# Performance work log

Measured on AMD Instinct MI355X. Metric: run time of the kernel, lower is better.

## Reference

```python
import jax, jax.numpy as jnp
import numpy as np


def setup_inputs() -> dict:
    key = jax.random.key(0)
    L, N, Q, C = 6, 64, 64, 256
    hs_pair = jax.random.normal(key, (L, N, Q, C), dtype=jnp.float32)
    return {"hs_pair": hs_pair}


def _merge_step(centers):
    # centers: [L, N, Q, C] -> [L, N, Q-1, C]
    L, N, Q, C = centers.shape
    # pairwise Euclidean distance via gram matrix (avoids [L,N,Q,Q,C] diff tensor)
    sq = jnp.sum(centers * centers, axis=-1)                      # [L,N,Q]
    gram = jnp.einsum('lnqc,lnpc->lnqp', centers, centers)        # [L,N,Q,Q]
    d2 = sq[..., :, None] + sq[..., None, :] - 2.0 * gram
    dist = jnp.sqrt(jnp.maximum(d2, 0.0))                         # [L,N,Q,Q]
    dist = dist + jnp.max(dist) * jnp.eye(Q, dtype=dist.dtype)
    idx = jnp.argmin(dist.reshape(L, N, Q * Q), axis=2)           # [L,N]
    x, y = idx // Q, idx % Q                                      # row-major argmin => x < y
    cx = jnp.take_along_axis(centers, x[:, :, None, None], axis=2)[:, :, 0]  # [L,N,C]
    cy = jnp.take_along_axis(centers, y[:, :, None, None], axis=2)[:, :, 0]  # [L,N,C]
    merged = (cx + cy) * 0.5
    last = centers[:, :, -1]                                      # [L,N,C]
    qr = jnp.arange(Q)
    mask_x = (qr[None, None, :] == x[:, :, None])[..., None]      # [L,N,Q,1]
    mask_y = (qr[None, None, :] == y[:, :, None])[..., None]
    centers = jnp.where(mask_x, merged[:, :, None, :], centers)
    centers = jnp.where(mask_y, last[:, :, None, :], centers)
    return centers[:, :, :-1]


def reference(hs_pair):
    centers = hs_pair
    Q0 = centers.shape[2]
    # Q-2 sequential merges; each iteration has a distinct static shape,
    # so a Python loop (unrolled under jit) is the correct structure.
    for _ in range(Q0 - 2):
        centers = _merge_step(centers)
    return centers  # [L, N, 2, C]
```

## Files before the change

### kernel.cpp

```cpp
#include <hip/hip_runtime.h>
#include <stdint.h>

#define NSLICE 384
#define QMAX   64
#define CDIM   256
#define NTHR   512

#define SW(r,c) ((r)*QMAX + ((c)^(r)))
#define INF_F  __int_as_float(0x7F800000)

__device__ __forceinline__ float dpp_sum64(float v) {
#define DPP_ADD(c) v += __int_as_float(__builtin_amdgcn_update_dpp(0, __float_as_int(v), c, 0xf, 0xf, true))
    DPP_ADD(0x111);
    DPP_ADD(0x112);
    DPP_ADD(0x114);
    DPP_ADD(0x118);
    DPP_ADD(0x142);
    DPP_ADD(0x143);
#undef DPP_ADD
    return v;
}

template<int CTRL>
__device__ __forceinline__ unsigned long long dpp_min64_step(unsigned long long v) {
    unsigned lo = (unsigned)v, hi = (unsigned)(v >> 32);
    unsigned olo = (unsigned)__builtin_amdgcn_update_dpp((int)lo, (int)lo, CTRL, 0xf, 0xf, false);
    unsigned ohi = (unsigned)__builtin_amdgcn_update_dpp((int)hi, (int)hi, CTRL, 0xf, 0xf, false);
    unsigned long long o = ((unsigned long long)ohi << 32) | olo;
    return o < v ? o : v;
}

__device__ __forceinline__ unsigned long long wave_min64_bcast(unsigned long long v) {
    v = dpp_min64_step<0x111>(v);
    v = dpp_min64_step<0x112>(v);
    v = dpp_min64_step<0x114>(v);
    v = dpp_min64_step<0x118>(v);
    v = dpp_min64_step<0x142>(v);
    v = dpp_min64_step<0x143>(v);
    unsigned lo = (unsigned)__builtin_amdgcn_readlane((int)(unsigned)v, 63);
    unsigned hi = (unsigned)__builtin_amdgcn_readlane((int)(unsigned)(v >> 32), 63);
    return ((unsigned long long)hi << 32) | lo;
}

__launch_bounds__(NTHR, 4)
__global__ void hca_kernel(const float* __restrict__ in, float* __restrict__ out) {
    __shared__ __align__(16) float cen[QMAX * CDIM];
    __shared__ __align__(16) float dist[QMAX * QMAX];

    const int tid  = threadIdx.x;
    const int lane = tid & 63;
    const int w    = tid >> 6;
    const int slice = blockIdx.x;
    const float* src = in + (size_t)slice * (QMAX * CDIM);
    float* dst = out + (size_t)slice * (2 * CDIM);

    {
        const float4* s4 = (const float4*)src;
        float4* c4 = (float4*)cen;
        #pragma unroll
        for (int i = 0; i < (QMAX * CDIM / 4) / NTHR; ++i)
            c4[tid + i * NTHR] = s4[tid + i * NTHR];
    }
    __syncthreads();

    {
        float4 A[8];
        #pragma unroll
        for (int r = 0; r < 8; ++r)
            A[r] = ((const float4*)(cen + (w + 8 * r) * CDIM))[lane];

        #pragma unroll
        for (int r = 0; r < 8; ++r) {
            float t = A[r].x * A[r].x;
            t = fmaf(A[r].y, A[r].y, t); t = fmaf(A[r].z, A[r].z, t); t = fmaf(A[r].w, A[r].w, t);
            float s = dpp_sum64(t);
            if (lane == 63) dist[(w + 8 * r) * QMAX] = s;
        }
        __syncthreads();

        float sqq[8];
        #pragma unroll
        for (int r = 0; r < 8; ++r) sqq[r] = dist[(w + 8 * r) * QMAX];
        for (int p = 1; p < QMAX; ++p) {
            const float4 b = ((const float4*)(cen + p * CDIM))[lane];
            const float sqp = dist[p * QMAX];
            #pragma unroll
            for (int r = 0; r < 8; ++r) {
                const int q = w + 8 * r;
                if (q < p) {
                    float t = A[r].x * b.x;
                    t = fmaf(A[r].y, b.y, t); t = fmaf(A[r].z, b.z, t); t = fmaf(A[r].w, b.w, t);
                    float s = dpp_sum64(t);
                    if (lane == 63) {
                        float d2 = sqq[r] + sqp - 2.0f * s;
                        float d  = sqrtf(fmaxf(d2, 0.0f));
                        dist[SW(q, p)] = d;
                        dist[SW(p, q)] = d;
                    }
                }
            }
        }
    }
    __syncthreads();

    if (w != 0) return;

    auto scan_chunk = [&](int i, unsigned long long& kmin) {
        const float4 dv = ((const float4*)dist)[i * 64 + lane];
        const int rr  = 4 * i + (lane >> 4);
        const int rb  = rr * 64;
        const int cc0 = (lane & 15) * 4;
        #pragma unroll
        for (int e = 0; e < 4; ++e) {
            unsigned long long kk =
                ((unsigned long long)__float_as_uint((&dv.x)[e]) << 32)
                | (unsigned)(rb + ((cc0 + e) ^ rr));
            kmin = kk < kmin ? kk : kmin;
        }
    };

    unsigned long long kmin = ~0ull;
    #pragma unroll
    for (int i = 0; i < 16; ++i) scan_chunk(i, kmin);
    kmin = wave_min64_bcast(kmin);

    for (int Q = QMAX; Q > 2; --Q) {
        const int Qm1 = Q - 1;
        const unsigned fl = (unsigned)kmin & 0xFFFu;
        const int x = (int)(fl >> 6), y = (int)(fl & 63);
        const float dxy = __uint_as_float((unsigned)(kmin >> 32));

        const float4 cx  = ((const float4*)(cen + x * CDIM))[lane];
        const float4 cy4 = ((const float4*)(cen + y * CDIM))[lane];
        const float4 cq  = ((const float4*)(cen + Qm1 * CDIM))[lane];

        const int p = lane;
        const bool act = (p < Qm1) && (p != x);
        const int p_old = (p == y) ? Qm1 : p;
        float dxp = 0.0f, dyp = 0.0f;
        if (act) { dxp = dist[SW(x, p_old)]; dyp = dist[SW(y, p_old)]; }
        const bool mv = (y != Qm1) && (p < Qm1) && (p != x) && (p != y);
        float rowQ1 = 0.0f, colQ1 = 0.0f;
        if (mv) { rowQ1 = dist[SW(Qm1, p)]; colQ1 = dist[SW(p, Qm1)]; }
        float t = 0.5f * (dxp * dxp + dyp * dyp) - 0.25f * (dxy * dxy);
        float d = sqrtf(fmaxf(t, 0.0f));
        if (mv) { dist[SW(y, p)] = rowQ1; dist[SW(p, y)] = colQ1; }
        if (p < Q) { dist[SW(Qm1, p)] = INF_F; dist[SW(p, Qm1)] = INF_F; }
        if (act) { dist[SW(x, p)] = d; dist[SW(p, x)] = d; }

        float4 m;
        m.x = (cx.x + cy4.x) * 0.5f; m.y = (cx.y + cy4.y) * 0.5f;
        m.z = (cx.z + cy4.z) * 0.5f; m.w = (cx.w + cy4.w) * 0.5f;
        ((float4*)(cen + x * CDIM))[lane] = m;
        if (y != Qm1) ((float4*)(cen + y * CDIM))[lane] = cq;

        if (Q > 3) {
            const int nc = ((Q - 2) >> 2) + 1;
            kmin = ~0ull;
            for (int i = 0; i < nc; ++i) scan_chunk(i, kmin);
            kmin = wave_min64_bcast(kmin);
        }
    }

    #pragma unroll
    for (int i = 0; i < 2; ++i)
        ((float4*)dst)[lane + 64 * i] = ((const float4*)cen)[lane + 64 * i];
}

extern "C" void kernel_launch(void* const* d_in, const int* in_sizes, int n_in,
                              void* d_out, int out_size, void* d_ws, size_t ws_size,
                              hipStream_t stream) {
    (void)in_sizes; (void)n_in; (void)d_ws; (void)ws_size; (void)out_size;
    const float* in = (const float*)d_in[0];
    float* out = (float*)d_out;
    hca_kernel<<<NSLICE, NTHR, 0, stream>>>(in, out);
}
```

Measured before the change: 147.2 us.

## Maintain per-row minimum keys incrementally instead of rescanning distance matrix

Replaces the full rescan of the remaining distance matrix after each merge with a per-lane row-minimum cache (one row per lane). After a merge, each row's cached minimum is patched for the row move and the new merged distances. Only rows whose cached minimum pointed at the removed or merged columns are rescanned, using wave-wide reductions. This cuts the per-step LDS scan work, at the cost of more complex bookkeeping and several extra cross-lane reductions per step.

```diff
diff --git a/kernel.cpp b/kernel.cpp
--- a/kernel.cpp
+++ b/kernel.cpp
@@ -8,6 +8,7 @@
 
 #define SW(r,c) ((r)*QMAX + ((c)^(r)))
 #define INF_F  __int_as_float(0x7F800000)
+typedef unsigned long long ull;
 
 __device__ __forceinline__ float dpp_sum64(float v) {
 #define DPP_ADD(c) v += __int_as_float(__builtin_amdgcn_update_dpp(0, __float_as_int(v), c, 0xf, 0xf, true))
@@ -22,15 +23,15 @@
 }
 
 template<int CTRL>
-__device__ __forceinline__ unsigned long long dpp_min64_step(unsigned long long v) {
+__device__ __forceinline__ ull dpp_min64_step(ull v) {
     unsigned lo = (unsigned)v, hi = (unsigned)(v >> 32);
     unsigned olo = (unsigned)__builtin_amdgcn_update_dpp((int)lo, (int)lo, CTRL, 0xf, 0xf, false);
     unsigned ohi = (unsigned)__builtin_amdgcn_update_dpp((int)hi, (int)hi, CTRL, 0xf, 0xf, false);
-    unsigned long long o = ((unsigned long long)ohi << 32) | olo;
+    ull o = ((ull)ohi << 32) | olo;
     return o < v ? o : v;
 }
 
-__device__ __forceinline__ unsigned long long wave_min64_bcast(unsigned long long v) {
+__device__ __forceinline__ ull wave_min64_bcast(ull v) {
     v = dpp_min64_step<0x111>(v);
     v = dpp_min64_step<0x112>(v);
     v = dpp_min64_step<0x114>(v);
@@ -39,7 +40,7 @@
     v = dpp_min64_step<0x143>(v);
     unsigned lo = (unsigned)__builtin_amdgcn_readlane((int)(unsigned)v, 63);
     unsigned hi = (unsigned)__builtin_amdgcn_readlane((int)(unsigned)(v >> 32), 63);
-    return ((unsigned long long)hi << 32) | lo;
+    return ((ull)hi << 32) | lo;
 }
 
 __launch_bounds__(NTHR, 4)
@@ -105,30 +106,38 @@
 
     if (w != 0) return;
 
-    auto scan_chunk = [&](int i, unsigned long long& kmin) {
-        const float4 dv = ((const float4*)dist)[i * 64 + lane];
-        const int rr  = 4 * i + (lane >> 4);
-        const int rb  = rr * 64;
-        const int cc0 = (lane & 15) * 4;
-        #pragma unroll
-        for (int e = 0; e < 4; ++e) {
-            unsigned long long kk =
-                ((unsigned long long)__float_as_uint((&dv.x)[e]) << 32)
-                | (unsigned)(rb + ((cc0 + e) ^ rr));
-            kmin = kk < kmin ? kk : kmin;
-        }
-    };
-
-    unsigned long long kmin = ~0ull;
-    #pragma unroll
-    for (int i = 0; i < 16; ++i) scan_chunk(i, kmin);
-    kmin = wave_min64_bcast(kmin);
+    unsigned khi, klo;
+    {
+        ull acc[8];
+        #pragma unroll
+        for (int i = 0; i < 8; ++i) acc[i] = ~0ull;
+        #pragma unroll
+        for (int j = 0; j < 8; ++j) {
+            #pragma unroll
+            for (int i = 0; i < 8; ++i) {
+                const int c = 8 * j + i;
+                unsigned b = __float_as_uint(dist[SW(lane, c)]);
+                ull kk = ((ull)b << 32) | (unsigned)((lane << 6) | c);
+                acc[i] = kk < acc[i] ? kk : acc[i];
+            }
+        }
+        acc[0] = acc[0] < acc[4] ? acc[0] : acc[4];
+        acc[1] = acc[1] < acc[5] ? acc[1] : acc[5];
+        acc[2] = acc[2] < acc[6] ? acc[2] : acc[6];
+        acc[3] = acc[3] < acc[7] ? acc[3] : acc[7];
+        acc[0] = acc[0] < acc[2] ? acc[0] : acc[2];
+        acc[1] = acc[1] < acc[3] ? acc[1] : acc[3];
+        ull key = acc[0] < acc[1] ? acc[0] : acc[1];
+        khi = (unsigned)(key >> 32); klo = (unsigned)key;
+    }
+    ull kmin = wave_min64_bcast(((ull)khi << 32) | klo);
 
     for (int Q = QMAX; Q > 2; --Q) {
         const int Qm1 = Q - 1;
         const unsigned fl = (unsigned)kmin & 0xFFFu;
         const int x = (int)(fl >> 6), y = (int)(fl & 63);
         const float dxy = __uint_as_float((unsigned)(kmin >> 32));
+        const bool has_mv = (y != Qm1);
 
         const float4 cx  = ((const float4*)(cen + x * CDIM))[lane];
         const float4 cy4 = ((const float4*)(cen + y * CDIM))[lane];
@@ -139,7 +148,7 @@
         const int p_old = (p == y) ? Qm1 : p;
         float dxp = 0.0f, dyp = 0.0f;
         if (act) { dxp = dist[SW(x, p_old)]; dyp = dist[SW(y, p_old)]; }
-        const bool mv = (y != Qm1) && (p < Qm1) && (p != x) && (p != y);
+        const bool mv = has_mv && (p < Qm1) && (p != x) && (p != y);
         float rowQ1 = 0.0f, colQ1 = 0.0f;
         if (mv) { rowQ1 = dist[SW(Qm1, p)]; colQ1 = dist[SW(p, Qm1)]; }
         float t = 0.5f * (dxp * dxp + dyp * dyp) - 0.25f * (dxy * dxy);
@@ -152,13 +161,43 @@
         m.x = (cx.x + cy4.x) * 0.5f; m.y = (cx.y + cy4.y) * 0.5f;
         m.z = (cx.z + cy4.z) * 0.5f; m.w = (cx.w + cy4.w) * 0.5f;
         ((float4*)(cen + x * CDIM))[lane] = m;
-        if (y != Qm1) ((float4*)(cen + y * CDIM))[lane] = cq;
+        if (has_mv) ((float4*)(cen + y * CDIM))[lane] = cq;
 
         if (Q > 3) {
-            const int nc = ((Q - 2) >> 2) + 1;
-            kmin = ~0ull;
-            for (int i = 0; i < nc; ++i) scan_chunk(i, kmin);
-            kmin = wave_min64_bcast(kmin);
+            const int Qn = Q - 1;
+            unsigned rawcol = klo & 63u;
+            bool stale = (rawcol == (unsigned)x) | (rawcol == (unsigned)y);
+            unsigned fixcol = (has_mv && rawcol == (unsigned)Qm1) ? (unsigned)y : rawcol;
+            const unsigned inh_hi  = (unsigned)__builtin_amdgcn_readlane((int)khi, Qm1);
+            const unsigned inh_raw = (unsigned)__builtin_amdgcn_readlane((int)rawcol, Qm1);
+            if (has_mv && p == y) {
+                khi = inh_hi;
+                fixcol = inh_raw;
+                stale = (inh_raw == (unsigned)x) | (inh_raw == (unsigned)y);
+            }
+            klo = (unsigned)(p << 6) | fixcol;
+            if (act && !stale) {
+                const unsigned db = __float_as_uint(d);
+                const unsigned cl = (unsigned)((p << 6) | x);
+                if ((db < khi) | ((db == khi) & (cl < klo))) { khi = db; klo = cl; }
+            }
+            {
+                const unsigned h = act ? __float_as_uint(d) : 0xFFFFFFFFu;
+                ull kx = ((ull)h << 32) | (unsigned)((x << 6) | p);
+                kx = wave_min64_bcast(kx);
+                if (p == x) { khi = (unsigned)(kx >> 32); klo = (unsigned)kx; }
+            }
+            if (p >= Qn) { khi = 0xFFFFFFFFu; klo = 0xFFFFFFFFu; }
+            ull smask = __ballot(stale && (p < Qn) && (p != x));
+            while (smask) {
+                const int r1 = (int)__builtin_ctzll(smask);
+                smask &= smask - 1;
+                unsigned b = __float_as_uint(dist[SW(r1, lane)]);
+                ull kk = ((ull)b << 32) | (unsigned)((r1 << 6) | lane);
+                kk = wave_min64_bcast(kk);
+                if (p == r1) { khi = (unsigned)(kk >> 32); klo = (unsigned)kk; }
+            }
+            kmin = wave_min64_bcast(((ull)khi << 32) | klo);
         }
     }
 
```

Result: slower. 437.9 us (+197.5%).

## Spread merge loop across all eight waves with shared-memory argmin reduction

Applied to the files above, without the earlier changes.

Instead of returning all waves but one after the distance matrix is built, the merge loop now keeps all eight waves alive. Wave 0 updates the distance rows while wave 1 updates the centroids in parallel. Each wave scans up to two chunks of the matrix and writes a partial min to scratch stored in row 63 of the dist array, and every wave reduces the eight partials. This shortens the serial scan per step, at the cost of two block-wide barriers per merge step and reduced occupancy for other blocks, since the block's waves no longer retire early.

```diff
diff --git a/kernel.cpp b/kernel.cpp
--- a/kernel.cpp
+++ b/kernel.cpp
@@ -8,6 +8,7 @@
 
 #define SW(r,c) ((r)*QMAX + ((c)^(r)))
 #define INF_F  __int_as_float(0x7F800000)
+typedef unsigned long long ull;
 
 __device__ __forceinline__ float dpp_sum64(float v) {
 #define DPP_ADD(c) v += __int_as_float(__builtin_amdgcn_update_dpp(0, __float_as_int(v), c, 0xf, 0xf, true))
@@ -22,30 +23,36 @@
 }
 
 template<int CTRL>
-__device__ __forceinline__ unsigned long long dpp_min64_step(unsigned long long v) {
+__device__ __forceinline__ ull dpp_min64_step(ull v) {
     unsigned lo = (unsigned)v, hi = (unsigned)(v >> 32);
     unsigned olo = (unsigned)__builtin_amdgcn_update_dpp((int)lo, (int)lo, CTRL, 0xf, 0xf, false);
     unsigned ohi = (unsigned)__builtin_amdgcn_update_dpp((int)hi, (int)hi, CTRL, 0xf, 0xf, false);
-    unsigned long long o = ((unsigned long long)ohi << 32) | olo;
+    ull o = ((ull)ohi << 32) | olo;
     return o < v ? o : v;
 }
 
-__device__ __forceinline__ unsigned long long wave_min64_bcast(unsigned long long v) {
+__device__ __forceinline__ ull wave_min64_lane63(ull v) {
     v = dpp_min64_step<0x111>(v);
     v = dpp_min64_step<0x112>(v);
     v = dpp_min64_step<0x114>(v);
     v = dpp_min64_step<0x118>(v);
     v = dpp_min64_step<0x142>(v);
     v = dpp_min64_step<0x143>(v);
+    return v;
+}
+
+__device__ __forceinline__ ull wave_min64_bcast(ull v) {
+    v = wave_min64_lane63(v);
     unsigned lo = (unsigned)__builtin_amdgcn_readlane((int)(unsigned)v, 63);
     unsigned hi = (unsigned)__builtin_amdgcn_readlane((int)(unsigned)(v >> 32), 63);
-    return ((unsigned long long)hi << 32) | lo;
+    return ((ull)hi << 32) | lo;
 }
 
 __launch_bounds__(NTHR, 4)
 __global__ void hca_kernel(const float* __restrict__ in, float* __restrict__ out) {
     __shared__ __align__(16) float cen[QMAX * CDIM];
     __shared__ __align__(16) float dist[QMAX * QMAX];
+    ull* const scratch = (ull*)(dist + 63 * QMAX);
 
     const int tid  = threadIdx.x;
     const int lane = tid & 63;
@@ -103,68 +110,107 @@
     }
     __syncthreads();
 
-    if (w != 0) return;
-
-    auto scan_chunk = [&](int i, unsigned long long& kmin) {
+    auto scan_chunk = [&](int i, ull& kmin) {
         const float4 dv = ((const float4*)dist)[i * 64 + lane];
         const int rr  = 4 * i + (lane >> 4);
         const int rb  = rr * 64;
         const int cc0 = (lane & 15) * 4;
         #pragma unroll
         for (int e = 0; e < 4; ++e) {
-            unsigned long long kk =
-                ((unsigned long long)__float_as_uint((&dv.x)[e]) << 32)
-                | (unsigned)(rb + ((cc0 + e) ^ rr));
+            ull kk = ((ull)__float_as_uint((&dv.x)[e]) << 32)
+                   | (unsigned)(rb + ((cc0 + e) ^ rr));
             kmin = kk < kmin ? kk : kmin;
         }
     };
 
-    unsigned long long kmin = ~0ull;
+    ull kmin0 = ~0ull;
     #pragma unroll
-    for (int i = 0; i < 16; ++i) scan_chunk(i, kmin);
-    kmin = wave_min64_bcast(kmin);
+    for (int i = 0; i < 16; ++i) scan_chunk(i, kmin0);
+    kmin0 = wave_min64_bcast(kmin0);
+    __syncthreads();
 
     for (int Q = QMAX; Q > 2; --Q) {
         const int Qm1 = Q - 1;
+
+        ull kmin;
+        if (Q == QMAX) {
+            kmin = kmin0;
+        } else {
+            ull s0 = scratch[0], s1 = scratch[1], s2 = scratch[2], s3 = scratch[3];
+            ull s4 = scratch[4], s5 = scratch[5], s6 = scratch[6], s7 = scratch[7];
+            ull a0 = s0 < s1 ? s0 : s1;
+            ull a1 = s2 < s3 ? s2 : s3;
+            ull a2 = s4 < s5 ? s4 : s5;
+            ull a3 = s6 < s7 ? s6 : s7;
+            a0 = a0 < a1 ? a0 : a1;
+            a2 = a2 < a3 ? a2 : a3;
+            kmin = a0 < a2 ? a0 : a2;
+        }
         const unsigned fl = (unsigned)kmin & 0xFFFu;
-        const int x = (int)(fl >> 6), y = (int)(fl & 63);
-        const float dxy = __uint_as_float((unsigned)(kmin >> 32));
-
-        const float4 cx  = ((const float4*)(cen + x * CDIM))[lane];
-        const float4 cy4 = ((const float4*)(cen + y * CDIM))[lane];
-        const float4 cq  = ((const float4*)(cen + Qm1 * CDIM))[lane];
-
-        const int p = lane;
-        const bool act = (p < Qm1) && (p != x);
-        const int p_old = (p == y) ? Qm1 : p;
-        float dxp = 0.0f, dyp = 0.0f;
-        if (act) { dxp = dist[SW(x, p_old)]; dyp = dist[SW(y, p_old)]; }
-        const bool mv = (y != Qm1) && (p < Qm1) && (p != x) && (p != y);
-        float rowQ1 = 0.0f, colQ1 = 0.0f;
-        if (mv) { rowQ1 = dist[SW(Qm1, p)]; colQ1 = dist[SW(p, Qm1)]; }
-        float t = 0.5f * (dxp * dxp + dyp * dyp) - 0.25f * (dxy * dxy);
-        float d = sqrtf(fmaxf(t, 0.0f));
-        if (mv) { dist[SW(y, p)] = rowQ1; dist[SW(p, y)] = colQ1; }
-        if (p < Q) { dist[SW(Qm1, p)] = INF_F; dist[SW(p, Qm1)] = INF_F; }
-        if (act) { dist[SW(x, p)] = d; dist[SW(p, x)] = d; }
-
-        float4 m;
-        m.x = (cx.x + cy4.x) * 0.5f; m.y = (cx.y + cy4.y) * 0.5f;
-        m.z = (cx.z + cy4.z) * 0.5f; m.w = (cx.w + cy4.w) * 0.5f;
-        ((float4*)(cen + x * CDIM))[lane] = m;
-        if (y != Qm1) ((float4*)(cen + y * CDIM))[lane] = cq;
+        const int x = __builtin_amdgcn_readfirstlane((int)(fl >> 6));
+        const int y = __builtin_amdgcn_readfirstlane((int)(fl & 63u));
+        const float dxy = __uint_as_float(
+            (unsigned)__builtin_amdgcn_readfirstlane((int)(unsigned)(kmin >> 32)));
+        const bool has_mv = (y != Qm1);
+
+        if (w == 0) {
+            const int p = lane;
+            const bool act = (p < Qm1) && (p != x);
+            const int p_old = (p == y) ? Qm1 : p;
+            float dxp = 0.0f, dyp = 0.0f;
+            if (act) { dxp = dist[SW(x, p_old)]; dyp = dist[SW(y, p_old)]; }
+            const bool mv = has_mv && (p < Qm1) && (p != x) && (p != y);
+            float rowQ1 = 0.0f, colQ1 = 0.0f;
+            if (mv) { rowQ1 = dist[SW(Qm1, p)]; colQ1 = dist[SW(p, Qm1)]; }
+            float t = 0.5f * (dxp * dxp + dyp * dyp) - 0.25f * (dxy * dxy);
+            float d = sqrtf(fmaxf(t, 0.0f));
+            if (mv) { dist[SW(y, p)] = rowQ1; dist[SW(p, y)] = colQ1; }
+            if (p < Q) { dist[SW(Qm1, p)] = INF_F; dist[SW(p, Qm1)] = INF_F; }
+            if (act) { dist[SW(x, p)] = d; dist[SW(p, x)] = d; }
+        }
+        if (w == 1) {
+            const float4 cx  = ((const float4*)(cen + x * CDIM))[lane];
+            const float4 cy4 = ((const float4*)(cen + y * CDIM))[lane];
+            const float4 cq  = ((const float4*)(cen + Qm1 * CDIM))[lane];
+            float4 m;
+            m.x = (cx.x + cy4.x) * 0.5f; m.y = (cx.y + cy4.y) * 0.5f;
+            m.z = (cx.z + cy4.z) * 0.5f; m.w = (cx.w + cy4.w) * 0.5f;
+            ((float4*)(cen + x * CDIM))[lane] = m;
+            if (has_mv) ((float4*)(cen + y * CDIM))[lane] = cq;
+        }
+        __syncthreads();
 
         if (Q > 3) {
-            const int nc = ((Q - 2) >> 2) + 1;
-            kmin = ~0ull;
-            for (int i = 0; i < nc; ++i) scan_chunk(i, kmin);
-            kmin = wave_min64_bcast(kmin);
-        }
+            const int Qs = Q - 1;
+            ull part = ~0ull;
+            const int c0 = w, c1 = w + 8;
+            if (4 * c0 < Qs) scan_chunk(c0, part);
+            if (4 * c1 < Qs) {
+                if (c1 == 15) {
+                    const float4 dv = ((const float4*)dist)[15 * 64 + lane];
+                    const int rr  = 60 + (lane >> 4);
+                    const int rb  = rr * 64;
+                    const int cc0 = (lane & 15) * 4;
+                    if (rr != 63) {
+                        #pragma unroll
+                        for (int e = 0; e < 4; ++e) {
+                            ull kk = ((ull)__float_as_uint((&dv.x)[e]) << 32)
+                                   | (unsigned)(rb + ((cc0 + e) ^ rr));
+                            part = kk < part ? kk : part;
+                        }
+                    }
+                } else {
+                    scan_chunk(c1, part);
+                }
+            }
+            part = wave_min64_lane63(part);
+            if (lane == 63) scratch[w] = part;
+        }
+        __syncthreads();
     }
 
-    #pragma unroll
-    for (int i = 0; i < 2; ++i)
-        ((float4*)dst)[lane + 64 * i] = ((const float4*)cen)[lane + 64 * i];
+    for (int i = tid; i < 2 * CDIM; i += NTHR)
+        dst[i] = cen[i];
 }
 
 extern "C" void kernel_launch(void* const* d_in, const int* in_sizes, int n_in,
```

New measurement: 144.5 us. No clear change (-1.9%).
